# Kernel tuning notes

Measured on AMD Instinct MI355X. Metric: run time of the kernel, lower is better.

Reference implementation:

```python
import jax, jax.numpy as jnp
import numpy as np

L1_WEIGHT = 0.5
SSIM_WEIGHT = 0.5
WINDOW_SIZE = 11
SIGMA = 1.5
C1 = 0.01 ** 2
C2 = 0.03 ** 2


def _gaussian_window(dtype):
    coords = jnp.arange(WINDOW_SIZE, dtype=dtype) - (WINDOW_SIZE // 2)
    g = jnp.exp(-(coords ** 2) / (2.0 * SIGMA ** 2))
    g = g / g.sum()
    return g[:, None] * g[None, :]  # (K, K)


def _depthwise_blur(x, win2d):
    # x: (B, C, H, W); depthwise conv with shared Gaussian kernel, SAME padding
    C = x.shape[1]
    kernel = jnp.broadcast_to(win2d[None, None], (C, 1, WINDOW_SIZE, WINDOW_SIZE))
    pad = WINDOW_SIZE // 2
    return jax.lax.conv_general_dilated(
        x, kernel,
        window_strides=(1, 1),
        padding=((pad, pad), (pad, pad)),
        dimension_numbers=("NCHW", "OIHW", "NCHW"),
        feature_group_count=C,
    )


def _ssim(img1, img2):
    win = _gaussian_window(img1.dtype)
    mu1 = _depthwise_blur(img1, win)
    mu2 = _depthwise_blur(img2, win)
    mu1_sq = mu1 * mu1
    mu2_sq = mu2 * mu2
    mu1_mu2 = mu1 * mu2
    sigma1_sq = _depthwise_blur(img1 * img1, win) - mu1_sq
    sigma2_sq = _depthwise_blur(img2 * img2, win) - mu2_sq
    sigma12 = _depthwise_blur(img1 * img2, win) - mu1_mu2
    ssim_map = ((2.0 * mu1_mu2 + C1) * (2.0 * sigma12 + C2)) / (
        (mu1_sq + mu2_sq + C1) * (sigma1_sq + sigma2_sq + C2)
    )
    return ssim_map.mean()


def setup_inputs() -> dict:
    key = jax.random.key(0)
    k1, k2 = jax.random.split(key)
    shape = (32, 3, 512, 512)
    warped = jax.random.uniform(k1, shape, dtype=jnp.float32)
    target = jax.random.uniform(k2, shape, dtype=jnp.float32)
    return {"warped": warped, "target": target}


def reference(warped, target):
    l1_loss = jnp.mean(jnp.abs(warped - target))
    ssim_val = _ssim(warped, target)
    ssim_loss = 1.0 - ssim_val
    total_loss = L1_WEIGHT * l1_loss + SSIM_WEIGHT * ssim_loss
    return total_loss
```

## Files before the change

### kernel.cpp

```cpp
#include <hip/hip_runtime.h>
#include <math.h>

#define IMW 512
#define IMH 512
#define NPIX (IMW * IMH)
#define NBX 8
#define NBY 16
#define NBLK (NBX * NBY * 96)
#define C1F 1.0e-4f
#define C2F 9.0e-4f
#define H2P 28
#define S0W 96
#define YW  4608

typedef short s16x8 __attribute__((ext_vector_type(8)));
typedef float f32x4 __attribute__((ext_vector_type(4)));

__device__ __forceinline__ unsigned cvtpk(float a, float b) {
    unsigned r;
    asm("v_cvt_pk_bf16_f32 %0, %1, %2" : "=v"(r) : "v"(a), "v"(b));
    return r;
}
__device__ __forceinline__ unsigned bf16_rne(float f) {
    unsigned u = __builtin_bit_cast(unsigned, f);
    return (u + 0x7FFFu + ((u >> 16) & 1u)) >> 16;
}
__device__ __forceinline__ float bf16_to_f(unsigned b) {
    return __builtin_bit_cast(float, b << 16);
}
__device__ __forceinline__ void gload16(const void* g, void* l) {
    __builtin_amdgcn_global_load_lds(
        (const __attribute__((address_space(1))) void*)g,
        (__attribute__((address_space(3))) void*)l,
        16, 0, 0);
}

__global__ void setup_kernel(uint4* __restrict__ wtab)
{
    const int lane = threadIdx.x;
    const int lane15 = lane & 15;
    const int g = lane >> 4;
    float w[11];
    float s = 0.f;
    for (int i = 0; i < 11; ++i) {
        const float c = (float)(i - 5);
        w[i] = expf(-(c * c) / 4.5f);
        s += w[i];
    }
    for (int i = 0; i < 11; ++i) w[i] /= s;

    s16x8 bwh, bwl, avh, avl;
    #pragma unroll
    for (int e = 0; e < 8; ++e) {
        const int k = 8 * g + e;
        const int th = k - lane15 - 3;
        const float wh = (th >= 0 && th <= 10) ? w[th] : 0.f;
        const int tv = k - lane15;
        const float wvv = (tv >= 0 && tv <= 10) ? w[tv] : 0.f;
        const unsigned h1 = bf16_rne(wh);
        const unsigned l1 = bf16_rne(wh - bf16_to_f(h1));
        bwh[e] = (short)h1; bwl[e] = (short)l1;
        const unsigned h2 = bf16_rne(wvv);
        const unsigned l2 = bf16_rne(wvv - bf16_to_f(h2));
        avh[e] = (short)h2; avl[e] = (short)l2;
    }
    wtab[lane * 4 + 0] = __builtin_bit_cast(uint4, bwh);
    wtab[lane * 4 + 1] = __builtin_bit_cast(uint4, bwl);
    wtab[lane * 4 + 2] = __builtin_bit_cast(uint4, avh);
    wtab[lane * 4 + 3] = __builtin_bit_cast(uint4, avl);
}

__global__ __launch_bounds__(256)
void ssim_l1_kernel(const float* __restrict__ warped,
                    const float* __restrict__ target,
                    const uint4* __restrict__ wtab,
                    float2* __restrict__ partial)
{
    __shared__ unsigned int LDSU[9224];

    const int tid = threadIdx.x;
    const int lane = tid & 63;
    const int wv = tid >> 6;
    const int lane15 = lane & 15;
    const int g = tid >> 4 & 3;
    const int c0 = blockIdx.x * 64;
    const int r0 = blockIdx.y * 32;
    const size_t base = (size_t)blockIdx.z * NPIX;
    char* LB = (char*)LDSU;

    {
        const char* xrow = (const char*)(warped + base);
        const char* yrow = (const char*)(target + base);
        const int cb0 = (c0 - 8) * 4;
        #pragma unroll
        for (int i = 0; i < 5; ++i) {
            const int ck = wv + 4 * i;
            if (ck < 18) {
                const unsigned off = 1024u * (unsigned)ck + 16u * (unsigned)lane;
                const unsigned q = off >> 7;
                const unsigned row = (q * 171u) >> 9;
                const unsigned rem = off - 384u * row;
                const unsigned gl = rem >> 4;
                const unsigned gs = gl ^ (row & 7u);
                const int srow = min(max(r0 - 5 + (int)row, 0), IMH - 1);
                const int scolb = min(max(cb0 + (int)(gs << 4), 0), 2032);
                const size_t rb = (size_t)srow * (IMW * 4);
                gload16(xrow + rb + scolb, LB + 1024 * ck);
                gload16(yrow + rb + scolb, LB + 18432 + 1024 * ck);
            }
        }
    }
    const s16x8 BwH = __builtin_bit_cast(s16x8, wtab[lane * 4 + 0]);
    const s16x8 BwL = __builtin_bit_cast(s16x8, wtab[lane * 4 + 1]);
    const s16x8 AvH = __builtin_bit_cast(s16x8, wtab[lane * 4 + 2]);
    const s16x8 AvL = __builtin_bit_cast(s16x8, wtab[lane * 4 + 3]);

    __syncthreads();

    if (blockIdx.y == 0) {
        #pragma unroll
        for (int k = tid; k < 960; k += 256)
            LDSU[(k < 480) ? k : (YW + k - 480)] = 0u;
    }
    if (blockIdx.y == NBY - 1) {
        #pragma unroll
        for (int k = tid; k < 960; k += 256)
            LDSU[(k < 480) ? (4128 + k) : (YW + 4128 + k - 480)] = 0u;
    }
    __syncthreads();

    const int s0 = 16 * wv + 8 * g;
    float colw[8];
    #pragma unroll
    for (int e = 0; e < 8; ++e) {
        const int s = s0 + e;
        colw[e] = (s < 8 || s > 71) ? 0.f : ((s < 16 || s >= 64) ? 1.f : 0.5f);
    }
    const bool xedge = (blockIdx.x == 0) || (blockIdx.x == NBX - 1);
    f32x4 mx0, mx1;
    #pragma unroll
    for (int e = 0; e < 4; ++e) {
        const int cA = c0 - 8 + s0 + e;
        const int cB = cA + 4;
        mx0[e] = (cA >= 0 && cA < IMW) ? 1.f : 0.f;
        mx1[e] = (cB >= 0 && cB < IMW) ? 1.f : 0.f;
    }

    float l1sum = 0.f;
    f32x4 C[4][3];
    #pragma unroll
    for (int q = 0; q < 4; ++q)
        #pragma unroll
        for (int T = 0; T < 3; ++T)
            C[q][T] = {0.f, 0.f, 0.f, 0.f};

    const unsigned wb = (unsigned)(s0 * 4);
    #pragma unroll
    for (int T = 0; T < 3; ++T) {
        const int rs = 16 * T + lane15;
        const unsigned rb = (unsigned)(rs * 384);
        const unsigned swz = (unsigned)((rs & 7) << 4);
        f32x4 x0 = *(const f32x4*)(LB + rb + (wb ^ swz));
        f32x4 x1 = *(const f32x4*)(LB + rb + ((wb + 16) ^ swz));
        f32x4 y0 = *(const f32x4*)(LB + 18432 + rb + (wb ^ swz));
        f32x4 y1 = *(const f32x4*)(LB + 18432 + rb + ((wb + 16) ^ swz));
        if (xedge) {
            x0 *= mx0; x1 *= mx1; y0 *= mx0; y1 *= mx1;
        }

        {
            const float rm = (T == 0) ? ((lane15 >= 5) ? 1.f : 0.f)
                           : (T == 1) ? 1.f
                           : ((lane15 <= 4) ? 1.f : 0.f);
            float acc = 0.f;
            #pragma unroll
            for (int e = 0; e < 4; ++e) acc = fmaf(colw[e], fabsf(x0[e] - y0[e]), acc);
            #pragma unroll
            for (int e = 0; e < 4; ++e) acc = fmaf(colw[4 + e], fabsf(x1[e] - y1[e]), acc);
            l1sum = fmaf(rm, acc, l1sum);
        }

        uint4 A0u, A1u, A2u, A3u;
        A0u.x = cvtpk(x0[0], x0[1]); A0u.y = cvtpk(x0[2], x0[3]);
        A0u.z = cvtpk(x1[0], x1[1]); A0u.w = cvtpk(x1[2], x1[3]);
        A1u.x = cvtpk(y0[0], y0[1]); A1u.y = cvtpk(y0[2], y0[3]);
        A1u.z = cvtpk(y1[0], y1[1]); A1u.w = cvtpk(y1[2], y1[3]);
        A2u.x = cvtpk(fmaf(x0[0], x0[0], y0[0] * y0[0]), fmaf(x0[1], x0[1], y0[1] * y0[1]));
        A2u.y = cvtpk(fmaf(x0[2], x0[2], y0[2] * y0[2]), fmaf(x0[3], x0[3], y0[3] * y0[3]));
        A2u.z = cvtpk(fmaf(x1[0], x1[0], y1[0] * y1[0]), fmaf(x1[1], x1[1], y1[1] * y1[1]));
        A2u.w = cvtpk(fmaf(x1[2], x1[2], y1[2] * y1[2]), fmaf(x1[3], x1[3], y1[3] * y1[3]));
        A3u.x = cvtpk(x0[0] * y0[0], x0[1] * y0[1]);
        A3u.y = cvtpk(x0[2] * y0[2], x0[3] * y0[3]);
        A3u.z = cvtpk(x1[0] * y1[0], x1[1] * y1[1]);
        A3u.w = cvtpk(x1[2] * y1[2], x1[3] * y1[3]);

        const s16x8 A0 = __builtin_bit_cast(s16x8, A0u);
        const s16x8 A1 = __builtin_bit_cast(s16x8, A1u);
        const s16x8 A2 = __builtin_bit_cast(s16x8, A2u);
        const s16x8 A3 = __builtin_bit_cast(s16x8, A3u);

        C[0][T] = __builtin_amdgcn_mfma_f32_16x16x32_bf16(A0, BwH, C[0][T], 0, 0, 0);
        C[0][T] = __builtin_amdgcn_mfma_f32_16x16x32_bf16(A0, BwL, C[0][T], 0, 0, 0);
        C[1][T] = __builtin_amdgcn_mfma_f32_16x16x32_bf16(A1, BwH, C[1][T], 0, 0, 0);
        C[1][T] = __builtin_amdgcn_mfma_f32_16x16x32_bf16(A1, BwL, C[1][T], 0, 0, 0);
        C[2][T] = __builtin_amdgcn_mfma_f32_16x16x32_bf16(A2, BwH, C[2][T], 0, 0, 0);
        C[2][T] = __builtin_amdgcn_mfma_f32_16x16x32_bf16(A2, BwL, C[2][T], 0, 0, 0);
        C[3][T] = __builtin_amdgcn_mfma_f32_16x16x32_bf16(A3, BwH, C[3][T], 0, 0, 0);
        C[3][T] = __builtin_amdgcn_mfma_f32_16x16x32_bf16(A3, BwL, C[3][T], 0, 0, 0);
    }
    __syncthreads();

    #pragma unroll
    for (int q = 0; q < 4; ++q) {
        #pragma unroll
        for (int T = 0; T < 3; ++T) {
            uint2 p;
            p.x = cvtpk(C[q][T][0], C[q][T][1]);
            p.y = cvtpk(C[q][T][2], C[q][T][3]);
            *(uint2*)&LDSU[((wv * 4 + q) * 16 + lane15) * H2P + 8 * T + 2 * g] = p;
        }
    }

    float ssum = 0.f;
    #pragma unroll
    for (int rbh = 0; rbh < 2; ++rbh) {
        f32x4 V[4];
        #pragma unroll
        for (int q = 0; q < 4; ++q) {
            const uint4 br = *(const uint4*)&LDSU[((wv * 4 + q) * 16 + lane15) * H2P + 8 * rbh + 4 * g];
            const s16x8 B = __builtin_bit_cast(s16x8, br);
            f32x4 acc = {0.f, 0.f, 0.f, 0.f};
            acc = __builtin_amdgcn_mfma_f32_16x16x32_bf16(AvH, B, acc, 0, 0, 0);
            acc = __builtin_amdgcn_mfma_f32_16x16x32_bf16(AvL, B, acc, 0, 0, 0);
            V[q] = acc;
        }
        #pragma unroll
        for (int r = 0; r < 4; ++r) {
            const float mu1 = V[0][r], mu2 = V[1][r];
            const float sq  = V[2][r], sxy = V[3][r];
            const float mu1sq = mu1 * mu1;
            const float mu2sq = mu2 * mu2;
            const float mu12  = mu1 * mu2;
            const float s12   = sxy - mu12;
            const float ssig  = sq - mu1sq - mu2sq;
            const float num = (2.f * mu12 + C1F) * (2.f * s12 + C2F);
            const float den = (mu1sq + mu2sq + C1F) * (ssig + C2F);
            ssum = fmaf(num, __builtin_amdgcn_rcpf(den), ssum);
        }
    }

    #pragma unroll
    for (int off = 32; off > 0; off >>= 1) {
        l1sum += __shfl_down(l1sum, off);
        ssum  += __shfl_down(ssum,  off);
    }
    float* red = (float*)&LDSU[9216];
    if (lane == 0) { red[wv] = l1sum; red[4 + wv] = ssum; }
    __syncthreads();
    if (tid == 0) {
        const float L1 = red[0] + red[1] + red[2] + red[3];
        const float SS = red[4] + red[5] + red[6] + red[7];
        const int bid = (blockIdx.z * gridDim.y + blockIdx.y) * gridDim.x + blockIdx.x;
        partial[bid] = make_float2(L1, SS);
    }
}

__global__ __launch_bounds__(256)
void reduce_kernel(const float2* __restrict__ partial, float* __restrict__ out)
{
    double l1 = 0.0, ss = 0.0;
    for (int i = threadIdx.x; i < NBLK; i += 256) {
        const float2 p = partial[i];
        l1 += (double)p.x;
        ss += (double)p.y;
    }
    #pragma unroll
    for (int off = 32; off > 0; off >>= 1) {
        l1 += __shfl_down(l1, off);
        ss += __shfl_down(ss, off);
    }
    __shared__ double red[8];
    const int wv = threadIdx.x >> 6, lane = threadIdx.x & 63;
    if (lane == 0) { red[wv] = l1; red[4 + wv] = ss; }
    __syncthreads();
    if (threadIdx.x == 0) {
        const double n = 25165824.0;
        const double L1 = (red[0] + red[1] + red[2] + red[3]) / n;
        const double SS = (red[4] + red[5] + red[6] + red[7]) / n;
        out[0] = (float)(0.5 * L1 + 0.5 * (1.0 - SS));
    }
}

extern "C" void kernel_launch(void* const* d_in, const int* in_sizes, int n_in,
                              void* d_out, int out_size, void* d_ws, size_t ws_size,
                              hipStream_t stream)
{
    const float* warped = (const float*)d_in[0];
    const float* target = (const float*)d_in[1];
    float* out = (float*)d_out;
    uint4* wtab = (uint4*)d_ws;
    float2* partial = (float2*)((char*)d_ws + 4096);

    hipLaunchKernelGGL(setup_kernel, dim3(1), dim3(64), 0, stream, wtab);
    hipLaunchKernelGGL(ssim_l1_kernel, dim3(NBX, NBY, 96), dim3(256), 0, stream,
                       warped, target, wtab, partial);
    hipLaunchKernelGGL(reduce_kernel, dim3(1), dim3(256), 0, stream, partial, out);
}
```

Measured before the change: 87.42 us.

## Use padded unswizzled LDS layout and mask border rows instead of zero-fill

Changes the LDS staging layout from a 384-byte XOR-swizzled pitch to a 336-byte padded pitch (21 chunks per row), so the loads take four uniform iterations with simpler index math and the total LDS footprint shrinks. The separate zero-fill pass for top and bottom image borders, along with its extra barrier, is removed; out-of-range rows are instead masked in registers on edge blocks. The elementwise L1 and SSIM arithmetic is also rewritten in vector form to encourage packed math. The risks are LDS bank conflicts with the new pitch and wider edge-path branching.

```diff
diff --git a/kernel.cpp b/kernel.cpp
--- a/kernel.cpp
+++ b/kernel.cpp
@@ -10,8 +10,8 @@
 #define C1F 1.0e-4f
 #define C2F 9.0e-4f
 #define H2P 28
-#define S0W 96
-#define YW  4608
+#define PITCH 336
+#define FOFF 16384
 
 typedef short s16x8 __attribute__((ext_vector_type(8)));
 typedef float f32x4 __attribute__((ext_vector_type(4)));
@@ -34,6 +34,7 @@
         (__attribute__((address_space(3))) void*)l,
         16, 0, 0);
 }
+__device__ __forceinline__ f32x4 spl4(float v) { f32x4 r = {v, v, v, v}; return r; }
 
 __global__ void setup_kernel(uint4* __restrict__ wtab)
 {
@@ -76,13 +77,13 @@
                     const uint4* __restrict__ wtab,
                     float2* __restrict__ partial)
 {
-    __shared__ unsigned int LDSU[9224];
+    __shared__ unsigned int LDSU[8192];
 
     const int tid = threadIdx.x;
     const int lane = tid & 63;
     const int wv = tid >> 6;
     const int lane15 = lane & 15;
-    const int g = tid >> 4 & 3;
+    const int g = (lane >> 4) & 3;
     const int c0 = blockIdx.x * 64;
     const int r0 = blockIdx.y * 32;
     const size_t base = (size_t)blockIdx.z * NPIX;
@@ -92,22 +93,18 @@
         const char* xrow = (const char*)(warped + base);
         const char* yrow = (const char*)(target + base);
         const int cb0 = (c0 - 8) * 4;
-        #pragma unroll
-        for (int i = 0; i < 5; ++i) {
+        const int gb = 64 * wv + lane;
+        #pragma unroll
+        for (int i = 0; i < 4; ++i) {
             const int ck = wv + 4 * i;
-            if (ck < 18) {
-                const unsigned off = 1024u * (unsigned)ck + 16u * (unsigned)lane;
-                const unsigned q = off >> 7;
-                const unsigned row = (q * 171u) >> 9;
-                const unsigned rem = off - 384u * row;
-                const unsigned gl = rem >> 4;
-                const unsigned gs = gl ^ (row & 7u);
-                const int srow = min(max(r0 - 5 + (int)row, 0), IMH - 1);
-                const int scolb = min(max(cb0 + (int)(gs << 4), 0), 2032);
-                const size_t rb = (size_t)srow * (IMW * 4);
-                gload16(xrow + rb + scolb, LB + 1024 * ck);
-                gload16(yrow + rb + scolb, LB + 18432 + 1024 * ck);
-            }
+            const unsigned G = (unsigned)(gb + 256 * i);
+            const unsigned row = (G * 3121u) >> 16;
+            const unsigned gl  = G - 21u * row;
+            const int srow = min(max(r0 - 5 + (int)row, 0), IMH - 1);
+            const int scolb = min(max(cb0 + (int)(gl << 4), 0), 2032);
+            const size_t rb = (size_t)srow * (IMW * 4);
+            gload16(xrow + rb + scolb, LB + 1024 * ck);
+            gload16(yrow + rb + scolb, LB + FOFF + 1024 * ck);
         }
     }
     const s16x8 BwH = __builtin_bit_cast(s16x8, wtab[lane * 4 + 0]);
@@ -117,82 +114,67 @@
 
     __syncthreads();
 
-    if (blockIdx.y == 0) {
-        #pragma unroll
-        for (int k = tid; k < 960; k += 256)
-            LDSU[(k < 480) ? k : (YW + k - 480)] = 0u;
-    }
-    if (blockIdx.y == NBY - 1) {
-        #pragma unroll
-        for (int k = tid; k < 960; k += 256)
-            LDSU[(k < 480) ? (4128 + k) : (YW + 4128 + k - 480)] = 0u;
-    }
-    __syncthreads();
-
     const int s0 = 16 * wv + 8 * g;
-    float colw[8];
-    #pragma unroll
-    for (int e = 0; e < 8; ++e) {
-        const int s = s0 + e;
-        colw[e] = (s < 8 || s > 71) ? 0.f : ((s < 16 || s >= 64) ? 1.f : 0.5f);
-    }
-    const bool xedge = (blockIdx.x == 0) || (blockIdx.x == NBX - 1);
-    f32x4 mx0, mx1;
+    f32x4 cw0, cw1, mx0, mx1;
     #pragma unroll
     for (int e = 0; e < 4; ++e) {
-        const int cA = c0 - 8 + s0 + e;
-        const int cB = cA + 4;
-        mx0[e] = (cA >= 0 && cA < IMW) ? 1.f : 0.f;
-        mx1[e] = (cB >= 0 && cB < IMW) ? 1.f : 0.f;
-    }
-
-    float l1sum = 0.f;
+        const int sA = s0 + e, sB = sA + 4;
+        cw0[e] = (sA < 8 || sA > 71) ? 0.f : ((sA < 16 || sA >= 64) ? 1.f : 0.5f);
+        cw1[e] = (sB < 8 || sB > 71) ? 0.f : ((sB < 16 || sB >= 64) ? 1.f : 0.5f);
+        const int cA = c0 - 8 + sA, cB = c0 - 8 + sB;
+        mx0[e] = ((unsigned)cA < (unsigned)IMW) ? 1.f : 0.f;
+        mx1[e] = ((unsigned)cB < (unsigned)IMW) ? 1.f : 0.f;
+    }
+    const bool edge = (blockIdx.x == 0) || (blockIdx.x == NBX - 1) ||
+                      (blockIdx.y == 0) || (blockIdx.y == NBY - 1);
+
+    f32x4 l1v = spl4(0.f);
     f32x4 C[4][3];
     #pragma unroll
     for (int q = 0; q < 4; ++q)
         #pragma unroll
         for (int T = 0; T < 3; ++T)
-            C[q][T] = {0.f, 0.f, 0.f, 0.f};
+            C[q][T] = spl4(0.f);
 
     const unsigned wb = (unsigned)(s0 * 4);
     #pragma unroll
     for (int T = 0; T < 3; ++T) {
         const int rs = 16 * T + lane15;
-        const unsigned rb = (unsigned)(rs * 384);
-        const unsigned swz = (unsigned)((rs & 7) << 4);
-        f32x4 x0 = *(const f32x4*)(LB + rb + (wb ^ swz));
-        f32x4 x1 = *(const f32x4*)(LB + rb + ((wb + 16) ^ swz));
-        f32x4 y0 = *(const f32x4*)(LB + 18432 + rb + (wb ^ swz));
-        f32x4 y1 = *(const f32x4*)(LB + 18432 + rb + ((wb + 16) ^ swz));
-        if (xedge) {
-            x0 *= mx0; x1 *= mx1; y0 *= mx0; y1 *= mx1;
+        const char* p = LB + rs * PITCH + wb;
+        f32x4 x0 = *(const f32x4*)p;
+        f32x4 x1 = *(const f32x4*)(p + 16);
+        f32x4 y0 = *(const f32x4*)(p + FOFF);
+        f32x4 y1 = *(const f32x4*)(p + FOFF + 16);
+        if (edge) {
+            const float rr = ((unsigned)(r0 - 5 + rs) < (unsigned)IMH) ? 1.f : 0.f;
+            const f32x4 m0 = mx0 * spl4(rr);
+            const f32x4 m1 = mx1 * spl4(rr);
+            x0 *= m0; x1 *= m1; y0 *= m0; y1 *= m1;
         }
 
         {
-            const float rm = (T == 0) ? ((lane15 >= 5) ? 1.f : 0.f)
-                           : (T == 1) ? 1.f
-                           : ((lane15 <= 4) ? 1.f : 0.f);
-            float acc = 0.f;
-            #pragma unroll
-            for (int e = 0; e < 4; ++e) acc = fmaf(colw[e], fabsf(x0[e] - y0[e]), acc);
-            #pragma unroll
-            for (int e = 0; e < 4; ++e) acc = fmaf(colw[4 + e], fabsf(x1[e] - y1[e]), acc);
-            l1sum = fmaf(rm, acc, l1sum);
-        }
+            const float rmL1 = (T == 0) ? ((lane15 >= 5) ? 1.f : 0.f)
+                             : (T == 1) ? 1.f
+                             : ((lane15 <= 4) ? 1.f : 0.f);
+            const f32x4 ad0 = __builtin_elementwise_abs(x0 - y0);
+            const f32x4 ad1 = __builtin_elementwise_abs(x1 - y1);
+            l1v = __builtin_elementwise_fma(cw0 * ad0 + cw1 * ad1, spl4(rmL1), l1v);
+        }
+
+        const f32x4 q2a = __builtin_elementwise_fma(x0, x0, y0 * y0);
+        const f32x4 q2b = __builtin_elementwise_fma(x1, x1, y1 * y1);
+        const f32x4 q3a = x0 * y0;
+        const f32x4 q3b = x1 * y1;
 
         uint4 A0u, A1u, A2u, A3u;
         A0u.x = cvtpk(x0[0], x0[1]); A0u.y = cvtpk(x0[2], x0[3]);
         A0u.z = cvtpk(x1[0], x1[1]); A0u.w = cvtpk(x1[2], x1[3]);
         A1u.x = cvtpk(y0[0], y0[1]); A1u.y = cvtpk(y0[2], y0[3]);
         A1u.z = cvtpk(y1[0], y1[1]); A1u.w = cvtpk(y1[2], y1[3]);
-        A2u.x = cvtpk(fmaf(x0[0], x0[0], y0[0] * y0[0]), fmaf(x0[1], x0[1], y0[1] * y0[1]));
-        A2u.y = cvtpk(fmaf(x0[2], x0[2], y0[2] * y0[2]), fmaf(x0[3], x0[3], y0[3] * y0[3]));
-        A2u.z = cvtpk(fmaf(x1[0], x1[0], y1[0] * y1[0]), fmaf(x1[1], x1[1], y1[1] * y1[1]));
-        A2u.w = cvtpk(fmaf(x1[2], x1[2], y1[2] * y1[2]), fmaf(x1[3], x1[3], y1[3] * y1[3]));
-        A3u.x = cvtpk(x0[0] * y0[0], x0[1] * y0[1]);
-        A3u.y = cvtpk(x0[2] * y0[2], x0[3] * y0[3]);
-        A3u.z = cvtpk(x1[0] * y1[0], x1[1] * y1[1]);
-        A3u.w = cvtpk(x1[2] * y1[2], x1[3] * y1[3]);
+        A2u.x = cvtpk(q2a[0], q2a[1]); A2u.y = cvtpk(q2a[2], q2a[3]);
+        A2u.z = cvtpk(q2b[0], q2b[1]); A2u.w = cvtpk(q2b[2], q2b[3]);
+        A3u.x = cvtpk(q3a[0], q3a[1]); A3u.y = cvtpk(q3a[2], q3a[3]);
+        A3u.z = cvtpk(q3b[0], q3b[1]); A3u.w = cvtpk(q3b[2], q3b[3]);
 
         const s16x8 A0 = __builtin_bit_cast(s16x8, A0u);
         const s16x8 A1 = __builtin_bit_cast(s16x8, A1u);
@@ -221,7 +203,7 @@
         }
     }
 
-    float ssum = 0.f;
+    f32x4 ssv = spl4(0.f);
     #pragma unroll
     for (int rbh = 0; rbh < 2; ++rbh) {
         f32x4 V[4];
@@ -229,32 +211,34 @@
         for (int q = 0; q < 4; ++q) {
             const uint4 br = *(const uint4*)&LDSU[((wv * 4 + q) * 16 + lane15) * H2P + 8 * rbh + 4 * g];
             const s16x8 B = __builtin_bit_cast(s16x8, br);
-            f32x4 acc = {0.f, 0.f, 0.f, 0.f};
+            f32x4 acc = spl4(0.f);
             acc = __builtin_amdgcn_mfma_f32_16x16x32_bf16(AvH, B, acc, 0, 0, 0);
             acc = __builtin_amdgcn_mfma_f32_16x16x32_bf16(AvL, B, acc, 0, 0, 0);
             V[q] = acc;
         }
-        #pragma unroll
-        for (int r = 0; r < 4; ++r) {
-            const float mu1 = V[0][r], mu2 = V[1][r];
-            const float sq  = V[2][r], sxy = V[3][r];
-            const float mu1sq = mu1 * mu1;
-            const float mu2sq = mu2 * mu2;
-            const float mu12  = mu1 * mu2;
-            const float s12   = sxy - mu12;
-            const float ssig  = sq - mu1sq - mu2sq;
-            const float num = (2.f * mu12 + C1F) * (2.f * s12 + C2F);
-            const float den = (mu1sq + mu2sq + C1F) * (ssig + C2F);
-            ssum = fmaf(num, __builtin_amdgcn_rcpf(den), ssum);
-        }
-    }
-
+        const f32x4 mu12  = V[0] * V[1];
+        const f32x4 mu1sq = V[0] * V[0];
+        const f32x4 mu2sq = V[1] * V[1];
+        const f32x4 s12   = V[3] - mu12;
+        const f32x4 ssig  = V[2] - mu1sq - mu2sq;
+        const f32x4 num = (spl4(2.f) * mu12 + spl4(C1F)) * (spl4(2.f) * s12 + spl4(C2F));
+        const f32x4 den = (mu1sq + mu2sq + spl4(C1F)) * (ssig + spl4(C2F));
+        f32x4 r;
+        r[0] = __builtin_amdgcn_rcpf(den[0]);
+        r[1] = __builtin_amdgcn_rcpf(den[1]);
+        r[2] = __builtin_amdgcn_rcpf(den[2]);
+        r[3] = __builtin_amdgcn_rcpf(den[3]);
+        ssv = __builtin_elementwise_fma(num, r, ssv);
+    }
+
+    float l1sum = (l1v[0] + l1v[1]) + (l1v[2] + l1v[3]);
+    float ssum  = (ssv[0] + ssv[1]) + (ssv[2] + ssv[3]);
     #pragma unroll
     for (int off = 32; off > 0; off >>= 1) {
         l1sum += __shfl_down(l1sum, off);
         ssum  += __shfl_down(ssum,  off);
     }
-    float* red = (float*)&LDSU[9216];
+    float* red = (float*)(LB + 32512);
     if (lane == 0) { red[wv] = l1sum; red[4 + wv] = ssum; }
     __syncthreads();
     if (tid == 0) {
```

Result: faster. 84.30 us (-3.6%).
